# Performance work log

Hardware: AMD Instinct MI355X
Metric: run time of the kernel (lower is better)

The kernel has to match this reference:

```python
import jax, jax.numpy as jnp
import numpy as np

B, N, D, H = 4, 2048, 256, 4
DH = D // H
EPS = 1e-5


def setup_inputs() -> dict:
    key = jax.random.key(0)
    ks = jax.random.split(key, 12)
    s = 0.02
    return {
        "x0": jax.random.normal(ks[0], (B, N, D), jnp.float32),
        "x1": jax.random.normal(ks[1], (B, N, D), jnp.float32),
        "w_qk": jax.random.normal(ks[2], (D, D), jnp.float32) * s,
        "b_qk": jax.random.normal(ks[3], (D,), jnp.float32) * s,
        "w_v": jax.random.normal(ks[4], (D, D), jnp.float32) * s,
        "b_v": jax.random.normal(ks[5], (D,), jnp.float32) * s,
        "w_out": jax.random.normal(ks[6], (D, D), jnp.float32) * s,
        "b_out": jax.random.normal(ks[7], (D,), jnp.float32) * s,
        "w_f1": jax.random.normal(ks[8], (2 * D, 2 * D), jnp.float32) * s,
        "b_f1": jax.random.normal(ks[9], (2 * D,), jnp.float32) * s,
        "ln_g": jnp.ones((2 * D,), jnp.float32),
        "ln_b": jnp.zeros((2 * D,), jnp.float32),
        "w_f2": jax.random.normal(ks[10], (2 * D, D), jnp.float32) * s,
        "b_f2": jax.random.normal(ks[11], (D,), jnp.float32) * s,
    }


def _split_heads(t):  # [b, n, h*d] -> [b, h, n, d]
    b, n, _ = t.shape
    return t.reshape(b, n, H, DH).transpose(0, 2, 1, 3)


def _merge_heads(t):  # [b, h, n, d] -> [b, n, h*d]
    b, h, n, d = t.shape
    return t.transpose(0, 2, 1, 3).reshape(b, n, h * d)


def _layernorm(x, g, b):
    mu = jnp.mean(x, axis=-1, keepdims=True)
    var = jnp.mean(jnp.square(x - mu), axis=-1, keepdims=True)
    return (x - mu) * jax.lax.rsqrt(var + EPS) * g + b


def reference(x0, x1, w_qk, b_qk, w_v, b_v, w_out, b_out,
              w_f1, b_f1, ln_g, ln_b, w_f2, b_f2):
    scale = DH ** -0.5
    qk0 = _split_heads(x0 @ w_qk + b_qk) * scale ** 0.5
    qk1 = _split_heads(x1 @ w_qk + b_qk) * scale ** 0.5
    v0 = _split_heads(x0 @ w_v + b_v)
    v1 = _split_heads(x1 @ w_v + b_v)

    # shared similarity matrix, bisoftmax: row-softmax for 0->1, col-softmax for 1->0
    sim = jnp.einsum('bhid,bhjd->bhij', qk0, qk1)  # [b,h,n0,n1]
    a0 = jax.nn.softmax(sim, axis=-1)              # over n1
    a1 = jax.nn.softmax(sim, axis=-2)              # over n0
    m0 = jnp.einsum('bhij,bhjd->bhid', a0, v1)     # [b,h,n0,d]
    m1 = jnp.einsum('bhji,bhjd->bhid', a1, v0)     # [b,h,n1,d]

    m0 = _merge_heads(m0) @ w_out + b_out
    m1 = _merge_heads(m1) @ w_out + b_out

    def ffn(x, m):
        h = jnp.concatenate([x, m], axis=-1) @ w_f1 + b_f1
        h = jax.nn.gelu(_layernorm(h, ln_g, ln_b), approximate=False)
        return x + h @ w_f2 + b_f2

    return ffn(x0, m0), ffn(x1, m1)
```

## Files before the change

kernel.cpp:

```cpp
#include <hip/hip_runtime.h>
#include <cstdint>
#include <cstddef>


#define QKS2 0.4246609001440095f

typedef short bf16x8 __attribute__((ext_vector_type(8)));
typedef float f32x4  __attribute__((ext_vector_type(4)));
typedef float f32x16 __attribute__((ext_vector_type(16)));

__device__ __forceinline__ uint16_t f2bf(float f){
  union { float f; uint32_t u; } v; v.f = f;
  uint32_t r = v.u + 0x7FFFu + ((v.u >> 16) & 1u);
  return (uint16_t)(r >> 16);
}
__device__ __forceinline__ uint16_t f2bf_trunc(float f){
  union { float f; uint32_t u; } v; v.f = f;
  return (uint16_t)(v.u >> 16);
}
__device__ __forceinline__ float bf2f(uint16_t h){
  union { uint32_t u; float f; } v; v.u = ((uint32_t)h) << 16; return v.f;
}

__device__ __forceinline__ void gl_lds16(const void* g, void* l){
  void* g2 = const_cast<void*>(g);
  __builtin_amdgcn_global_load_lds((__attribute__((address_space(1))) void*)g2,
                                   (__attribute__((address_space(3))) void*)l,
                                   16, 0, 0);
}

__global__ __launch_bounds__(256) void conv_x_k(const float* __restrict__ x0,
                                                const float* __restrict__ x1,
                                                uint16_t* __restrict__ xb){
  const float* src = blockIdx.z ? x1 : x0;
  uint16_t* dst = xb + (size_t)blockIdx.z * 2097152;
  size_t i = ((size_t)blockIdx.x * 256 + threadIdx.x) * 4;
  float4 v = *(const float4*)(src + i);
  uint2 o;
  o.x = (uint32_t)f2bf(v.x) | ((uint32_t)f2bf(v.y) << 16);
  o.y = (uint32_t)f2bf(v.z) | ((uint32_t)f2bf(v.w) << 16);
  *(uint2*)(dst + i) = o;
}

__global__ __launch_bounds__(256) void conv_w_k(
    const float* w0, const float* w1, const float* w2, const float* w3, const float* w4,
    uint16_t* t0, uint16_t* t1, uint16_t* t2, uint16_t* t3, uint16_t* t4){
  const int z = blockIdx.z;
  const float* src = z==0? w0 : z==1? w1 : z==2? w2 : z==3? w3 : w4;
  uint16_t*   dst  = z==0? t0 : z==1? t1 : z==2? t2 : z==3? t3 : t4;
  const int K = (z>=3)? 512 : 256;
  const int N = (z==3)? 512 : 256;
  int idx = blockIdx.x * 256 + threadIdx.x;
  if (idx >= (K*N)/4) return;
  int k = idx / (N/4);
  int n = (idx % (N/4)) * 4;
  float4 v = *(const float4*)(src + (size_t)k*N + n);
  dst[(size_t)(n+0)*K + k] = f2bf(v.x);
  dst[(size_t)(n+1)*K + k] = f2bf(v.y);
  dst[(size_t)(n+2)*K + k] = f2bf(v.z);
  dst[(size_t)(n+3)*K + k] = f2bf(v.w);
}

struct GemmArgs {
  const uint16_t* A0; const uint16_t* A1;
  const uint16_t* A2_0; const uint16_t* A2_1;
  const uint16_t* Wt0; const uint16_t* Wt1;
  const float* bias0; const float* bias1;
  uint16_t* out0; uint16_t* out1; uint16_t* out2; uint16_t* out3;
  float* fout; const float* xf0; const float* xf1;
  int K;
};

template<int MODE>
__global__ __launch_bounds__(256, 4) void gemm_k(GemmArgs a){
  __shared__ __align__(16) uint16_t As[64*64];
  __shared__ __align__(16) uint16_t Bs[128*64];
  const int tid = threadIdx.x;
  const int w = tid >> 6, l = tid & 63;
  const int z = blockIdx.z;
  const int which = (MODE==0) ? (z & 1) : z;
  const int wsel  = (MODE==0) ? (z >> 1) : 0;
  const int K = a.K;
  const int m0 = blockIdx.x * 64;
  const int n0 = blockIdx.y * 128;
  const uint16_t* Wt   = wsel ? a.Wt1 : a.Wt0;
  const float* bias    = wsel ? a.bias1 : a.bias0;
  const uint16_t* Ab   = which ? a.A1 : a.A0;
  const uint16_t* Ab2  = which ? a.A2_1 : a.A2_0;

  f32x4 acc[4][2];
  #pragma unroll
  for (int i=0;i<4;++i)
    #pragma unroll
    for (int j=0;j<2;++j) acc[i][j] = (f32x4){0.f,0.f,0.f,0.f};

  const int lrow8 = l >> 3, lch = l & 7;
  const int swch = (lch ^ lrow8) * 8;
  const int quad = l >> 4, l15 = l & 15, h7 = l15 & 7;

  for (int k0 = 0; k0 < K; k0 += 64){
    __syncthreads();
    const uint16_t* Asrc; int lda;
    if (MODE == 2){
      Asrc = (k0 < 256) ? (Ab + k0) : (Ab2 + (k0 - 256));
      lda = 256;
    } else { Asrc = Ab + k0; lda = K; }
    #pragma unroll
    for (int j=0;j<2;++j){
      int wi = w*2 + j;
      int row = wi*8 + lrow8;
      gl_lds16(Asrc + (size_t)(m0 + row)*lda + swch, &As[wi*512]);
    }
    #pragma unroll
    for (int j=0;j<4;++j){
      int wi = w*4 + j;
      int row = wi*8 + lrow8;
      gl_lds16(Wt + (size_t)(n0 + row)*K + k0 + swch, &Bs[wi*512]);
    }
    __syncthreads();
    #pragma unroll
    for (int kc=0;kc<2;++kc){
      const int fch = ((kc*4 + quad) ^ h7) * 8;
      bf16x8 af[4], bfr[2];
      #pragma unroll
      for (int rt=0;rt<4;++rt)
        af[rt] = *(const bf16x8*)&As[(rt*16 + l15)*64 + fch];
      #pragma unroll
      for (int ct=0;ct<2;++ct)
        bfr[ct] = *(const bf16x8*)&Bs[(w*32 + ct*16 + l15)*64 + fch];
      #pragma unroll
      for (int rt=0;rt<4;++rt)
        #pragma unroll
        for (int ct=0;ct<2;++ct)
          acc[rt][ct] = __builtin_amdgcn_mfma_f32_16x16x32_bf16(af[rt], bfr[ct], acc[rt][ct], 0,0,0);
    }
  }

  #pragma unroll
  for (int rt=0;rt<4;++rt){
    const int r0 = m0 + rt*16 + (quad<<2);
    #pragma unroll
    for (int ct=0;ct<2;++ct){
      const int c = n0 + w*32 + ct*16 + l15;
      const float bv = bias[c];
      if (MODE == 0){
        if (wsel == 0){
          uint16_t* q = which ? a.out1 : a.out0;
          #pragma unroll
          for (int i=0;i<4;++i)
            q[(size_t)(r0+i)*256 + c] = f2bf((acc[rt][ct][i] + bv) * QKS2);
        } else {
          uint16_t* vt = which ? a.out3 : a.out2;
          const int bb = r0 >> 11, nn = r0 & 2047;
          const int hh = c >> 6,  dd = c & 63;
          uint2 pk;
          pk.x = (uint32_t)f2bf(acc[rt][ct][0] + bv) | ((uint32_t)f2bf(acc[rt][ct][1] + bv) << 16);
          pk.y = (uint32_t)f2bf(acc[rt][ct][2] + bv) | ((uint32_t)f2bf(acc[rt][ct][3] + bv) << 16);
          *(uint2*)(vt + ((size_t)((bb*4 + hh)*64 + dd))*2048 + nn) = pk;
        }
      } else if (MODE == 1){
        uint16_t* o = which ? a.out1 : a.out0;
        #pragma unroll
        for (int i=0;i<4;++i)
          o[(size_t)(r0+i)*256 + c] = f2bf(acc[rt][ct][i] + bv);
      } else if (MODE == 2){
        uint16_t* o = which ? a.out1 : a.out0;
        #pragma unroll
        for (int i=0;i<4;++i)
          o[(size_t)(r0+i)*512 + c] = f2bf(acc[rt][ct][i] + bv);
      } else {
        const float* xf = which ? a.xf1 : a.xf0;
        float* fo = a.fout + (size_t)which * 2097152;
        #pragma unroll
        for (int i=0;i<4;++i)
          fo[(size_t)(r0+i)*256 + c] = acc[rt][ct][i] + bv + xf[(size_t)(r0+i)*256 + c];
      }
    }
  }
}

__global__ __launch_bounds__(128, 2) void flash_k(
    const uint16_t* __restrict__ qk0, const uint16_t* __restrict__ qk1,
    const uint16_t* __restrict__ vt0, const uint16_t* __restrict__ vt1,
    uint16_t* __restrict__ m0b, uint16_t* __restrict__ m1b){
  __shared__ __align__(16) uint16_t Ks[64*64];
  __shared__ __align__(16) uint16_t Vs[64*64];
  __shared__ __align__(16) uint16_t Ps[64*64];
  const int tid = threadIdx.x;
  const int w = tid >> 6, l = tid & 63;
  const int qt = blockIdx.x;
  const int bh = blockIdx.y;
  const int dir = blockIdx.z;
  const int b = bh >> 2, h = bh & 3;
  const uint16_t* Q   = dir ? qk1 : qk0;
  const uint16_t* Kg  = dir ? qk0 : qk1;
  const uint16_t* Vt  = dir ? vt0 : vt1;
  uint16_t* outp      = dir ? m1b : m0b;

  const int qrow0 = b*2048 + qt*64;
  const int lrow8 = l >> 3, lch = l & 7;
  const int l31 = l & 31, lhi = l >> 5;
  const int rsub = l31 >> 3;

  const short ONE = (short)0x3F80;
  const bf16x8 ones = {ONE,ONE,ONE,ONE,ONE,ONE,ONE,ONE};

  #pragma unroll
  for (int j=0;j<4;++j){
    int g = w*4 + j;
    int row = g*8 + lrow8;
    int sc = (lch ^ lrow8 ^ (g & 7)) * 8;
    gl_lds16(Q + (size_t)(qrow0 + row)*256 + h*64 + sc, &Ps[g*512]);
  }
  __syncthreads();
  bf16x8 qf[4];
  {
    const int qmask = (l & 7) ^ ((w*4 + rsub) & 7);
    #pragma unroll
    for (int ks=0;ks<4;++ks){
      int ch = (ks*2 + lhi) ^ qmask;
      qf[ks] = *(const bf16x8*)&Ps[(w*32 + l31)*64 + ch*8];
    }
  }

  f32x16 o0, o1, lacc;
  #pragma unroll
  for (int i=0;i<16;++i){ o0[i]=0.f; o1[i]=0.f; lacc[i]=0.f; }

  const size_t vbase = (size_t)bh * 64 * 2048;
  const int pmask = (l & 7) ^ ((w*4 + rsub) & 7);

  for (int kt=0; kt<32; ++kt){
    __syncthreads();
    #pragma unroll
    for (int j=0;j<4;++j){
      int g = w*4 + j;
      int row = g*8 + lrow8;
      int sc = (lch ^ lrow8 ^ (g & 7)) * 8;
      gl_lds16(Kg + (size_t)(b*2048 + kt*64 + row)*256 + h*64 + sc, &Ks[g*512]);
      gl_lds16(Vt + vbase + (size_t)row*2048 + kt*64 + sc, &Vs[g*512]);
    }
    __syncthreads();

    f32x16 s0, s1;
    #pragma unroll
    for (int i=0;i<16;++i){ s0[i]=0.f; s1[i]=0.f; }
    #pragma unroll
    for (int ks=0;ks<4;++ks){
      int ch0 = ((ks*2 + lhi) ^ (l & 7) ^ rsub) * 8;
      int ch1 = ((ks*2 + lhi) ^ (l & 7) ^ (4 + rsub)) * 8;
      bf16x8 k0 = *(const bf16x8*)&Ks[l31*64 + ch0];
      bf16x8 k1 = *(const bf16x8*)&Ks[(32 + l31)*64 + ch1];
      s0 = __builtin_amdgcn_mfma_f32_32x32x16_bf16(qf[ks], k0, s0, 0,0,0);
      s1 = __builtin_amdgcn_mfma_f32_32x32x16_bf16(qf[ks], k1, s1, 0,0,0);
    }

    #pragma unroll
    for (int reg=0; reg<16; ++reg){
      int rm   = (reg&3) + 8*(reg>>2) + 4*lhi;
      int row  = w*32 + rm;
      int mask = ((rm & 7) ^ ((w*4 + (reg>>2)) & 7));
      int kc0  = (l31 >> 3);
      float p0 = __builtin_amdgcn_exp2f(s0[reg]);
      Ps[row*64 + ((kc0 ^ mask))*8 + (l31 & 7)] = f2bf_trunc(p0);
      float p1 = __builtin_amdgcn_exp2f(s1[reg]);
      Ps[row*64 + (((4 + kc0) ^ mask))*8 + (l31 & 7)] = f2bf_trunc(p1);
    }

    bf16x8 pf[4];
    #pragma unroll
    for (int ks=0;ks<4;++ks){
      int ch = ((ks*2 + lhi) ^ pmask) * 8;
      pf[ks] = *(const bf16x8*)&Ps[(w*32 + l31)*64 + ch];
    }
    #pragma unroll
    for (int ks=0;ks<4;++ks)
      lacc = __builtin_amdgcn_mfma_f32_32x32x16_bf16(pf[ks], ones, lacc, 0,0,0);
    #pragma unroll
    for (int ks=0;ks<4;++ks){
      int ch0 = ((ks*2 + lhi) ^ (l & 7) ^ rsub) * 8;
      int ch1 = ((ks*2 + lhi) ^ (l & 7) ^ (4 + rsub)) * 8;
      bf16x8 v0 = *(const bf16x8*)&Vs[l31*64 + ch0];
      bf16x8 v1 = *(const bf16x8*)&Vs[(32 + l31)*64 + ch1];
      o0 = __builtin_amdgcn_mfma_f32_32x32x16_bf16(pf[ks], v0, o0, 0,0,0);
      o1 = __builtin_amdgcn_mfma_f32_32x32x16_bf16(pf[ks], v1, o1, 0,0,0);
    }
  }

  const int c0 = h*64 + l31;
  #pragma unroll
  for (int reg=0; reg<16; ++reg){
    float inv = 1.0f / lacc[reg];
    int rm  = (reg&3) + 8*(reg>>2) + 4*lhi;
    size_t row = (size_t)(qrow0 + w*32 + rm);
    outp[row*256 + c0]      = f2bf(o0[reg] * inv);
    outp[row*256 + c0 + 32] = f2bf(o1[reg] * inv);
  }
}

__global__ __launch_bounds__(256) void lngelu_k(const uint16_t* __restrict__ hpre,
                                                const float* __restrict__ g,
                                                const float* __restrict__ bb,
                                                uint16_t* __restrict__ h){
  const int row = blockIdx.x*4 + (threadIdx.x >> 6);
  const int l = threadIdx.x & 63;
  const uint16_t* rp = hpre + (size_t)row*512 + l*8;
  uint4 raw = *(const uint4*)rp;
  uint32_t wv[4] = {raw.x, raw.y, raw.z, raw.w};
  float x[8];
  #pragma unroll
  for (int j=0;j<4;++j){
    x[2*j]   = bf2f((uint16_t)(wv[j] & 0xFFFFu));
    x[2*j+1] = bf2f((uint16_t)(wv[j] >> 16));
  }
  float s = 0.f;
  #pragma unroll
  for (int j=0;j<8;++j) s += x[j];
  #pragma unroll
  for (int off=1; off<64; off<<=1) s += __shfl_xor(s, off, 64);
  float mu = s * (1.0f/512.0f);
  float vs = 0.f;
  #pragma unroll
  for (int j=0;j<8;++j){ float d = x[j]-mu; vs += d*d; }
  #pragma unroll
  for (int off=1; off<64; off<<=1) vs += __shfl_xor(vs, off, 64);
  float rstd = rsqrtf(vs*(1.0f/512.0f) + 1e-5f);
  const float* gp = g + l*8;
  const float* bp = bb + l*8;
  uint32_t ow[4];
  #pragma unroll
  for (int j=0;j<4;++j){
    float y0 = (x[2*j]-mu)*rstd*gp[2*j] + bp[2*j];
    float y1 = (x[2*j+1]-mu)*rstd*gp[2*j+1] + bp[2*j+1];
    float g0 = 0.5f*y0*(1.0f + erff(y0*0.70710678118f));
    float g1 = 0.5f*y1*(1.0f + erff(y1*0.70710678118f));
    ow[j] = (uint32_t)f2bf(g0) | ((uint32_t)f2bf(g1) << 16);
  }
  uint4 out4 = {ow[0], ow[1], ow[2], ow[3]};
  *(uint4*)(h + (size_t)row*512 + l*8) = out4;
}

extern "C" void kernel_launch(void* const* d_in, const int* in_sizes, int n_in,
                              void* d_out, int out_size, void* d_ws, size_t ws_size,
                              hipStream_t stream){
  (void)in_sizes; (void)n_in; (void)out_size; (void)ws_size;
  const float* x0   = (const float*)d_in[0];
  const float* x1   = (const float*)d_in[1];
  const float* w_qk = (const float*)d_in[2];
  const float* b_qk = (const float*)d_in[3];
  const float* w_v  = (const float*)d_in[4];
  const float* b_v  = (const float*)d_in[5];
  const float* w_out= (const float*)d_in[6];
  const float* b_out= (const float*)d_in[7];
  const float* w_f1 = (const float*)d_in[8];
  const float* b_f1 = (const float*)d_in[9];
  const float* ln_g = (const float*)d_in[10];
  const float* ln_b = (const float*)d_in[11];
  const float* w_f2 = (const float*)d_in[12];
  const float* b_f2 = (const float*)d_in[13];

  char* ws = (char*)d_ws;
  uint16_t* xb    = (uint16_t*)(ws);
  uint16_t* wqkT  = (uint16_t*)(ws +  8388608);
  uint16_t* wvT   = (uint16_t*)(ws +  8519680);
  uint16_t* woutT = (uint16_t*)(ws +  8650752);
  uint16_t* wf1T  = (uint16_t*)(ws +  8781824);
  uint16_t* wf2T  = (uint16_t*)(ws +  9306112);
  uint16_t* qk0b  = (uint16_t*)(ws +  9568256);
  uint16_t* qk1b  = (uint16_t*)(ws + 13762560);
  uint16_t* vt0b  = (uint16_t*)(ws + 17956864);
  uint16_t* vt1b  = (uint16_t*)(ws + 22151168);
  uint16_t* m0b   = (uint16_t*)(ws + 26345472);
  uint16_t* m1b   = (uint16_t*)(ws + 30539776);
  uint16_t* mp0b  = (uint16_t*)(ws + 34734080);
  uint16_t* mp1b  = (uint16_t*)(ws + 38928384);
  uint16_t* hpreb = qk0b;
  uint16_t* hb    = m0b;

  conv_x_k<<<dim3(2048,1,2), 256, 0, stream>>>(x0, x1, xb);
  conv_w_k<<<dim3(256,1,5), 256, 0, stream>>>(w_qk, w_v, w_out, w_f1, w_f2,
                                              wqkT, wvT, woutT, wf1T, wf2T);

  GemmArgs g0 = {};
  g0.A0 = xb; g0.A1 = xb + 2097152;
  g0.Wt0 = wqkT; g0.Wt1 = wvT;
  g0.bias0 = b_qk; g0.bias1 = b_v;
  g0.out0 = qk0b; g0.out1 = qk1b; g0.out2 = vt0b; g0.out3 = vt1b;
  g0.K = 256;
  gemm_k<0><<<dim3(128,2,4), 256, 0, stream>>>(g0);

  flash_k<<<dim3(32,16,2), 128, 0, stream>>>(qk0b, qk1b, vt0b, vt1b, m0b, m1b);

  GemmArgs g1 = {};
  g1.A0 = m0b; g1.A1 = m1b;
  g1.Wt0 = woutT; g1.bias0 = b_out;
  g1.out0 = mp0b; g1.out1 = mp1b;
  g1.K = 256;
  gemm_k<1><<<dim3(128,2,2), 256, 0, stream>>>(g1);

  GemmArgs g2 = {};
  g2.A0 = xb; g2.A1 = xb + 2097152;
  g2.A2_0 = mp0b; g2.A2_1 = mp1b;
  g2.Wt0 = wf1T; g2.bias0 = b_f1;
  g2.out0 = hpreb; g2.out1 = hpreb + 4194304;
  g2.K = 512;
  gemm_k<2><<<dim3(128,4,2), 256, 0, stream>>>(g2);

  lngelu_k<<<dim3(4096,1,1), 256, 0, stream>>>(hpreb, ln_g, ln_b, hb);

  GemmArgs g3 = {};
  g3.A0 = hb; g3.A1 = hb + 4194304;
  g3.Wt0 = wf2T; g3.bias0 = b_f2;
  g3.fout = (float*)d_out;
  g3.xf0 = x0; g3.xf1 = x1;
  g3.K = 512;
  gemm_k<3><<<dim3(128,2,2), 256, 0, stream>>>(g3);
}
```

Baseline: 221.8 us.

## Compute transposed S^T in flash kernel, keep P in registers via bpermute, drop LDS

The attention kernel now computes S^T = K·Q^T so each lane holds scores for its own query column. The probabilities are repacked into MFMA operand fragments with ds_bpermute in place of a round trip through shared memory, and O^T is accumulated as V^T·P^T. K and V tiles are loaded straight from global memory into registers, with no LDS staging and no __syncthreads. This removes LDS traffic and barriers, but every wave now loads K/V itself with no sharing across the block, and the 16-byte gathers are strided.

```diff
diff --git a/kernel.cpp b/kernel.cpp
--- a/kernel.cpp
+++ b/kernel.cpp
@@ -14,12 +14,14 @@
   uint32_t r = v.u + 0x7FFFu + ((v.u >> 16) & 1u);
   return (uint16_t)(r >> 16);
 }
-__device__ __forceinline__ uint16_t f2bf_trunc(float f){
-  union { float f; uint32_t u; } v; v.f = f;
-  return (uint16_t)(v.u >> 16);
-}
 __device__ __forceinline__ float bf2f(uint16_t h){
   union { uint32_t u; float f; } v; v.u = ((uint32_t)h) << 16; return v.f;
+}
+__device__ __forceinline__ uint32_t fbits(float f){
+  union { float f; uint32_t u; } v; v.f = f; return v.u;
+}
+__device__ __forceinline__ uint32_t pk2bf(float a, float b){
+  return (fbits(b) & 0xFFFF0000u) | (fbits(a) >> 16);
 }
 
 __device__ __forceinline__ void gl_lds16(const void* g, void* l){
@@ -183,11 +185,9 @@
     const uint16_t* __restrict__ qk0, const uint16_t* __restrict__ qk1,
     const uint16_t* __restrict__ vt0, const uint16_t* __restrict__ vt1,
     uint16_t* __restrict__ m0b, uint16_t* __restrict__ m1b){
-  __shared__ __align__(16) uint16_t Ks[64*64];
-  __shared__ __align__(16) uint16_t Vs[64*64];
-  __shared__ __align__(16) uint16_t Ps[64*64];
   const int tid = threadIdx.x;
   const int w = tid >> 6, l = tid & 63;
+  const int l31 = l & 31, lhi = l >> 5;
   const int qt = blockIdx.x;
   const int bh = blockIdx.y;
   const int dir = blockIdx.z;
@@ -197,104 +197,105 @@
   const uint16_t* Vt  = dir ? vt0 : vt1;
   uint16_t* outp      = dir ? m1b : m0b;
 
-  const int qrow0 = b*2048 + qt*64;
-  const int lrow8 = l >> 3, lch = l & 7;
-  const int l31 = l & 31, lhi = l >> 5;
-  const int rsub = l31 >> 3;
+  const int qrow = b*2048 + qt*64 + w*32 + l31;
+  const int pidx = (l ^ 32) << 2;
+  const bool hi = (lhi != 0);
 
   const short ONE = (short)0x3F80;
   const bf16x8 ones = {ONE,ONE,ONE,ONE,ONE,ONE,ONE,ONE};
 
-  #pragma unroll
-  for (int j=0;j<4;++j){
-    int g = w*4 + j;
-    int row = g*8 + lrow8;
-    int sc = (lch ^ lrow8 ^ (g & 7)) * 8;
-    gl_lds16(Q + (size_t)(qrow0 + row)*256 + h*64 + sc, &Ps[g*512]);
-  }
-  __syncthreads();
   bf16x8 qf[4];
   {
-    const int qmask = (l & 7) ^ ((w*4 + rsub) & 7);
+    const uint16_t* qp = Q + (size_t)qrow*256 + h*64 + lhi*8;
+    #pragma unroll
+    for (int ks=0;ks<4;++ks) qf[ks] = *(const bf16x8*)(qp + ks*16);
+  }
+
+  f32x16 o0, o1, lacc;
+  #pragma unroll
+  for (int i=0;i<16;++i){ o0[i]=0.f; o1[i]=0.f; lacc[i]=0.f; }
+
+  const uint16_t* Kbase = Kg + (size_t)(b*2048 + l31)*256 + h*64 + lhi*8;
+  const uint16_t* Vbase = Vt + (size_t)bh*131072 + (size_t)l31*2048 + lhi*8;
+
+  for (int kt=0; kt<32; ++kt){
+    bf16x8 kf[2][4], vf[2][4];
+    #pragma unroll
+    for (int kb=0;kb<2;++kb)
+      #pragma unroll
+      for (int ks=0;ks<4;++ks)
+        kf[kb][ks] = *(const bf16x8*)(Kbase + (size_t)(kt*64 + kb*32)*256 + ks*16);
+    #pragma unroll
+    for (int db=0;db<2;++db)
+      #pragma unroll
+      for (int ks=0;ks<4;++ks)
+        vf[db][ks] = *(const bf16x8*)(Vbase + (size_t)db*32*2048 + kt*64 + ks*16);
+
+    f32x16 st0, st1;
+    #pragma unroll
+    for (int i=0;i<16;++i){ st0[i]=0.f; st1[i]=0.f; }
     #pragma unroll
     for (int ks=0;ks<4;++ks){
-      int ch = (ks*2 + lhi) ^ qmask;
-      qf[ks] = *(const bf16x8*)&Ps[(w*32 + l31)*64 + ch*8];
-    }
-  }
-
-  f32x16 o0, o1, lacc;
-  #pragma unroll
-  for (int i=0;i<16;++i){ o0[i]=0.f; o1[i]=0.f; lacc[i]=0.f; }
-
-  const size_t vbase = (size_t)bh * 64 * 2048;
-  const int pmask = (l & 7) ^ ((w*4 + rsub) & 7);
-
-  for (int kt=0; kt<32; ++kt){
-    __syncthreads();
-    #pragma unroll
-    for (int j=0;j<4;++j){
-      int g = w*4 + j;
-      int row = g*8 + lrow8;
-      int sc = (lch ^ lrow8 ^ (g & 7)) * 8;
-      gl_lds16(Kg + (size_t)(b*2048 + kt*64 + row)*256 + h*64 + sc, &Ks[g*512]);
-      gl_lds16(Vt + vbase + (size_t)row*2048 + kt*64 + sc, &Vs[g*512]);
-    }
-    __syncthreads();
-
-    f32x16 s0, s1;
-    #pragma unroll
-    for (int i=0;i<16;++i){ s0[i]=0.f; s1[i]=0.f; }
-    #pragma unroll
-    for (int ks=0;ks<4;++ks){
-      int ch0 = ((ks*2 + lhi) ^ (l & 7) ^ rsub) * 8;
-      int ch1 = ((ks*2 + lhi) ^ (l & 7) ^ (4 + rsub)) * 8;
-      bf16x8 k0 = *(const bf16x8*)&Ks[l31*64 + ch0];
-      bf16x8 k1 = *(const bf16x8*)&Ks[(32 + l31)*64 + ch1];
-      s0 = __builtin_amdgcn_mfma_f32_32x32x16_bf16(qf[ks], k0, s0, 0,0,0);
-      s1 = __builtin_amdgcn_mfma_f32_32x32x16_bf16(qf[ks], k1, s1, 0,0,0);
-    }
-
-    #pragma unroll
-    for (int reg=0; reg<16; ++reg){
-      int rm   = (reg&3) + 8*(reg>>2) + 4*lhi;
-      int row  = w*32 + rm;
-      int mask = ((rm & 7) ^ ((w*4 + (reg>>2)) & 7));
-      int kc0  = (l31 >> 3);
-      float p0 = __builtin_amdgcn_exp2f(s0[reg]);
-      Ps[row*64 + ((kc0 ^ mask))*8 + (l31 & 7)] = f2bf_trunc(p0);
-      float p1 = __builtin_amdgcn_exp2f(s1[reg]);
-      Ps[row*64 + (((4 + kc0) ^ mask))*8 + (l31 & 7)] = f2bf_trunc(p1);
-    }
-
-    bf16x8 pf[4];
-    #pragma unroll
-    for (int ks=0;ks<4;++ks){
-      int ch = ((ks*2 + lhi) ^ pmask) * 8;
-      pf[ks] = *(const bf16x8*)&Ps[(w*32 + l31)*64 + ch];
-    }
-    #pragma unroll
-    for (int ks=0;ks<4;++ks)
-      lacc = __builtin_amdgcn_mfma_f32_32x32x16_bf16(pf[ks], ones, lacc, 0,0,0);
-    #pragma unroll
-    for (int ks=0;ks<4;++ks){
-      int ch0 = ((ks*2 + lhi) ^ (l & 7) ^ rsub) * 8;
-      int ch1 = ((ks*2 + lhi) ^ (l & 7) ^ (4 + rsub)) * 8;
-      bf16x8 v0 = *(const bf16x8*)&Vs[l31*64 + ch0];
-      bf16x8 v1 = *(const bf16x8*)&Vs[(32 + l31)*64 + ch1];
-      o0 = __builtin_amdgcn_mfma_f32_32x32x16_bf16(pf[ks], v0, o0, 0,0,0);
-      o1 = __builtin_amdgcn_mfma_f32_32x32x16_bf16(pf[ks], v1, o1, 0,0,0);
-    }
-  }
-
-  const int c0 = h*64 + l31;
-  #pragma unroll
-  for (int reg=0; reg<16; ++reg){
-    float inv = 1.0f / lacc[reg];
-    int rm  = (reg&3) + 8*(reg>>2) + 4*lhi;
-    size_t row = (size_t)(qrow0 + w*32 + rm);
-    outp[row*256 + c0]      = f2bf(o0[reg] * inv);
-    outp[row*256 + c0 + 32] = f2bf(o1[reg] * inv);
+      st0 = __builtin_amdgcn_mfma_f32_32x32x16_bf16(kf[0][ks], qf[ks], st0, 0,0,0);
+      st1 = __builtin_amdgcn_mfma_f32_32x32x16_bf16(kf[1][ks], qf[ks], st1, 0,0,0);
+    }
+
+    uint32_t pkA[2][4], pkB[2][4];
+    #pragma unroll
+    for (int g=0; g<4; ++g){
+      float a0 = __builtin_amdgcn_exp2f(st0[4*g+0]);
+      float a1 = __builtin_amdgcn_exp2f(st0[4*g+1]);
+      float a2 = __builtin_amdgcn_exp2f(st0[4*g+2]);
+      float a3 = __builtin_amdgcn_exp2f(st0[4*g+3]);
+      pkA[0][g] = pk2bf(a0, a1);
+      pkB[0][g] = pk2bf(a2, a3);
+      float c0 = __builtin_amdgcn_exp2f(st1[4*g+0]);
+      float c1 = __builtin_amdgcn_exp2f(st1[4*g+1]);
+      float c2 = __builtin_amdgcn_exp2f(st1[4*g+2]);
+      float c3 = __builtin_amdgcn_exp2f(st1[4*g+3]);
+      pkA[1][g] = pk2bf(c0, c1);
+      pkB[1][g] = pk2bf(c2, c3);
+    }
+
+    bf16x8 pfrag[4];
+    #pragma unroll
+    for (int f=0; f<4; ++f){
+      const int sb = f >> 1, m2 = f & 1;
+      uint32_t ownA0 = pkA[sb][2*m2],   ownB0 = pkB[sb][2*m2];
+      uint32_t ownA1 = pkA[sb][2*m2+1], ownB1 = pkB[sb][2*m2+1];
+      uint32_t tA = hi ? ownA0 : ownA1;
+      uint32_t tB = hi ? ownB0 : ownB1;
+      uint32_t rA = (uint32_t)__builtin_amdgcn_ds_bpermute(pidx, (int)tA);
+      uint32_t rB = (uint32_t)__builtin_amdgcn_ds_bpermute(pidx, (int)tB);
+      uint32_t v0 = hi ? rA : ownA0;
+      uint32_t v1 = hi ? rB : ownB0;
+      uint32_t v2 = hi ? ownA1 : rA;
+      uint32_t v3 = hi ? ownB1 : rB;
+      union { uint32_t u[4]; bf16x8 v; } cvt;
+      cvt.u[0]=v0; cvt.u[1]=v1; cvt.u[2]=v2; cvt.u[3]=v3;
+      pfrag[f] = cvt.v;
+    }
+
+    #pragma unroll
+    for (int f=0; f<4; ++f)
+      lacc = __builtin_amdgcn_mfma_f32_32x32x16_bf16(ones, pfrag[f], lacc, 0,0,0);
+    #pragma unroll
+    for (int f=0; f<4; ++f){
+      o0 = __builtin_amdgcn_mfma_f32_32x32x16_bf16(vf[0][f], pfrag[f], o0, 0,0,0);
+      o1 = __builtin_amdgcn_mfma_f32_32x32x16_bf16(vf[1][f], pfrag[f], o1, 0,0,0);
+    }
+  }
+
+  const float inv = 1.0f / lacc[0];
+  uint16_t* op = outp + (size_t)qrow*256 + h*64 + lhi*4;
+  #pragma unroll
+  for (int g=0; g<4; ++g){
+    uint32_t p01 = (uint32_t)f2bf(o0[4*g+0]*inv) | ((uint32_t)f2bf(o0[4*g+1]*inv) << 16);
+    uint32_t p23 = (uint32_t)f2bf(o0[4*g+2]*inv) | ((uint32_t)f2bf(o0[4*g+3]*inv) << 16);
+    *(uint2*)(op + 8*g) = (uint2){p01, p23};
+    uint32_t q01 = (uint32_t)f2bf(o1[4*g+0]*inv) | ((uint32_t)f2bf(o1[4*g+1]*inv) << 16);
+    uint32_t q23 = (uint32_t)f2bf(o1[4*g+2]*inv) | ((uint32_t)f2bf(o1[4*g+3]*inv) << 16);
+    *(uint2*)(op + 32 + 8*g) = (uint2){q01, q23};
   }
 }
 
```

Result: slower. 299.7 us (+35.1%).

## Double K-tile depth in GEMM and flash kernels, merge conversion launches

Applied to the files above, without the earlier changes.

The GEMM now stages 128-wide K slices per iteration with a 16-chunk XOR swizzle, which halves the number of barrier-separated load/compute rounds, and its occupancy hint drops from 4 to 3 blocks. The flash kernel processes 128 keys per tile, computing four 32-key score blocks and then running one fused P·V and row-sum loop, so it has half as many sync rounds. The x and weight conversion kernels become a single launch with seven z-slices. In exchange LDS use per block rises, which may lower occupancy, and the conversion grid launches many idle weight blocks that exit early.

```diff
diff --git a/kernel.cpp b/kernel.cpp
--- a/kernel.cpp
+++ b/kernel.cpp
@@ -29,23 +29,23 @@
                                    16, 0, 0);
 }
 
-__global__ __launch_bounds__(256) void conv_x_k(const float* __restrict__ x0,
-                                                const float* __restrict__ x1,
-                                                uint16_t* __restrict__ xb){
-  const float* src = blockIdx.z ? x1 : x0;
-  uint16_t* dst = xb + (size_t)blockIdx.z * 2097152;
-  size_t i = ((size_t)blockIdx.x * 256 + threadIdx.x) * 4;
-  float4 v = *(const float4*)(src + i);
-  uint2 o;
-  o.x = (uint32_t)f2bf(v.x) | ((uint32_t)f2bf(v.y) << 16);
-  o.y = (uint32_t)f2bf(v.z) | ((uint32_t)f2bf(v.w) << 16);
-  *(uint2*)(dst + i) = o;
-}
-
-__global__ __launch_bounds__(256) void conv_w_k(
+__global__ __launch_bounds__(256) void conv_all_k(
+    const float* __restrict__ x0, const float* __restrict__ x1,
+    uint16_t* __restrict__ xb,
     const float* w0, const float* w1, const float* w2, const float* w3, const float* w4,
     uint16_t* t0, uint16_t* t1, uint16_t* t2, uint16_t* t3, uint16_t* t4){
   const int z = blockIdx.z;
+  if (z >= 5){
+    const float* src = (z == 6) ? x1 : x0;
+    uint16_t* dst = xb + (size_t)(z - 5) * 2097152;
+    size_t i = ((size_t)blockIdx.x * 256 + threadIdx.x) * 4;
+    float4 v = *(const float4*)(src + i);
+    uint2 o;
+    o.x = (uint32_t)f2bf(v.x) | ((uint32_t)f2bf(v.y) << 16);
+    o.y = (uint32_t)f2bf(v.z) | ((uint32_t)f2bf(v.w) << 16);
+    *(uint2*)(dst + i) = o;
+    return;
+  }
   const float* src = z==0? w0 : z==1? w1 : z==2? w2 : z==3? w3 : w4;
   uint16_t*   dst  = z==0? t0 : z==1? t1 : z==2? t2 : z==3? t3 : t4;
   const int K = (z>=3)? 512 : 256;
@@ -72,9 +72,9 @@
 };
 
 template<int MODE>
-__global__ __launch_bounds__(256, 4) void gemm_k(GemmArgs a){
-  __shared__ __align__(16) uint16_t As[64*64];
-  __shared__ __align__(16) uint16_t Bs[128*64];
+__global__ __launch_bounds__(256, 3) void gemm_k(GemmArgs a){
+  __shared__ __align__(16) uint16_t As[64*128];
+  __shared__ __align__(16) uint16_t Bs[128*128];
   const int tid = threadIdx.x;
   const int w = tid >> 6, l = tid & 63;
   const int z = blockIdx.z;
@@ -94,11 +94,10 @@
     #pragma unroll
     for (int j=0;j<2;++j) acc[i][j] = (f32x4){0.f,0.f,0.f,0.f};
 
-  const int lrow8 = l >> 3, lch = l & 7;
-  const int swch = (lch ^ lrow8) * 8;
-  const int quad = l >> 4, l15 = l & 15, h7 = l15 & 7;
-
-  for (int k0 = 0; k0 < K; k0 += 64){
+  const int lrow16 = l >> 4, lch16 = l & 15;
+  const int quad = l >> 4, l15 = l & 15;
+
+  for (int k0 = 0; k0 < K; k0 += 128){
     __syncthreads();
     const uint16_t* Asrc; int lda;
     if (MODE == 2){
@@ -106,28 +105,30 @@
       lda = 256;
     } else { Asrc = Ab + k0; lda = K; }
     #pragma unroll
-    for (int j=0;j<2;++j){
-      int wi = w*2 + j;
-      int row = wi*8 + lrow8;
-      gl_lds16(Asrc + (size_t)(m0 + row)*lda + swch, &As[wi*512]);
-    }
-    #pragma unroll
     for (int j=0;j<4;++j){
-      int wi = w*4 + j;
-      int row = wi*8 + lrow8;
-      gl_lds16(Wt + (size_t)(n0 + row)*K + k0 + swch, &Bs[wi*512]);
+      int g = w*4 + j;
+      int row = g*4 + lrow16;
+      int sc = lch16 ^ (row & 15);
+      gl_lds16(Asrc + (size_t)(m0 + row)*lda + sc*8, &As[g*512]);
+    }
+    #pragma unroll
+    for (int j=0;j<8;++j){
+      int g = w*8 + j;
+      int row = g*4 + lrow16;
+      int sc = lch16 ^ (row & 15);
+      gl_lds16(Wt + (size_t)(n0 + row)*K + k0 + sc*8, &Bs[g*512]);
     }
     __syncthreads();
     #pragma unroll
-    for (int kc=0;kc<2;++kc){
-      const int fch = ((kc*4 + quad) ^ h7) * 8;
+    for (int kc=0;kc<4;++kc){
+      const int ch = kc*4 + quad;
       bf16x8 af[4], bfr[2];
       #pragma unroll
       for (int rt=0;rt<4;++rt)
-        af[rt] = *(const bf16x8*)&As[(rt*16 + l15)*64 + fch];
+        af[rt] = *(const bf16x8*)&As[(rt*16 + l15)*128 + (ch ^ l15)*8];
       #pragma unroll
       for (int ct=0;ct<2;++ct)
-        bfr[ct] = *(const bf16x8*)&Bs[(w*32 + ct*16 + l15)*64 + fch];
+        bfr[ct] = *(const bf16x8*)&Bs[(w*32 + ct*16 + l15)*128 + (ch ^ l15)*8];
       #pragma unroll
       for (int rt=0;rt<4;++rt)
         #pragma unroll
@@ -183,11 +184,13 @@
     const uint16_t* __restrict__ qk0, const uint16_t* __restrict__ qk1,
     const uint16_t* __restrict__ vt0, const uint16_t* __restrict__ vt1,
     uint16_t* __restrict__ m0b, uint16_t* __restrict__ m1b){
-  __shared__ __align__(16) uint16_t Ks[64*64];
-  __shared__ __align__(16) uint16_t Vs[64*64];
-  __shared__ __align__(16) uint16_t Ps[64*64];
+  __shared__ __align__(16) uint16_t Ks[128*64];
+  __shared__ __align__(16) uint16_t Vs[64*128];
+  __shared__ __align__(16) uint16_t Ps[64*128];
   const int tid = threadIdx.x;
   const int w = tid >> 6, l = tid & 63;
+  const int l31 = l & 31, lhi = l >> 5;
+  const int rsub = l31 >> 3;
   const int qt = blockIdx.x;
   const int bh = blockIdx.y;
   const int dir = blockIdx.z;
@@ -198,9 +201,8 @@
   uint16_t* outp      = dir ? m1b : m0b;
 
   const int qrow0 = b*2048 + qt*64;
-  const int lrow8 = l >> 3, lch = l & 7;
-  const int l31 = l & 31, lhi = l >> 5;
-  const int rsub = l31 >> 3;
+  const int lrow8 = l >> 3, lch8 = l & 7;
+  const int lrow16 = l >> 4, lch16 = l & 15;
 
   const short ONE = (short)0x3F80;
   const bf16x8 ones = {ONE,ONE,ONE,ONE,ONE,ONE,ONE,ONE};
@@ -209,81 +211,70 @@
   for (int j=0;j<4;++j){
     int g = w*4 + j;
     int row = g*8 + lrow8;
-    int sc = (lch ^ lrow8 ^ (g & 7)) * 8;
-    gl_lds16(Q + (size_t)(qrow0 + row)*256 + h*64 + sc, &Ps[g*512]);
+    int sc = lch8 ^ lrow8 ^ (g & 7);
+    gl_lds16(Q + (size_t)(qrow0 + row)*256 + h*64 + sc*8, &Ps[g*512]);
   }
   __syncthreads();
   bf16x8 qf[4];
   {
     const int qmask = (l & 7) ^ ((w*4 + rsub) & 7);
     #pragma unroll
-    for (int ks=0;ks<4;++ks){
-      int ch = (ks*2 + lhi) ^ qmask;
-      qf[ks] = *(const bf16x8*)&Ps[(w*32 + l31)*64 + ch*8];
-    }
+    for (int ks=0;ks<4;++ks)
+      qf[ks] = *(const bf16x8*)&Ps[(w*32 + l31)*64 + (((ks*2 + lhi) ^ qmask))*8];
   }
 
   f32x16 o0, o1, lacc;
   #pragma unroll
   for (int i=0;i<16;++i){ o0[i]=0.f; o1[i]=0.f; lacc[i]=0.f; }
 
-  const size_t vbase = (size_t)bh * 64 * 2048;
-  const int pmask = (l & 7) ^ ((w*4 + rsub) & 7);
-
-  for (int kt=0; kt<32; ++kt){
+  const size_t vbase = (size_t)bh * 131072;
+  const int pm15 = l31 & 15;
+
+  for (int kt=0; kt<16; ++kt){
     __syncthreads();
     #pragma unroll
-    for (int j=0;j<4;++j){
-      int g = w*4 + j;
-      int row = g*8 + lrow8;
-      int sc = (lch ^ lrow8 ^ (g & 7)) * 8;
-      gl_lds16(Kg + (size_t)(b*2048 + kt*64 + row)*256 + h*64 + sc, &Ks[g*512]);
-      gl_lds16(Vt + vbase + (size_t)row*2048 + kt*64 + sc, &Vs[g*512]);
+    for (int j=0;j<8;++j){
+      int g = w*8 + j;
+      int rowk = g*8 + lrow8;
+      int sck = lch8 ^ lrow8 ^ (g & 7);
+      gl_lds16(Kg + (size_t)(b*2048 + kt*128 + rowk)*256 + h*64 + sck*8, &Ks[g*512]);
+      int rowv = g*4 + lrow16;
+      int scv = lch16 ^ (rowv & 15);
+      gl_lds16(Vt + vbase + (size_t)rowv*2048 + kt*128 + scv*8, &Vs[g*1024]);
     }
     __syncthreads();
 
-    f32x16 s0, s1;
-    #pragma unroll
-    for (int i=0;i<16;++i){ s0[i]=0.f; s1[i]=0.f; }
-    #pragma unroll
-    for (int ks=0;ks<4;++ks){
-      int ch0 = ((ks*2 + lhi) ^ (l & 7) ^ rsub) * 8;
-      int ch1 = ((ks*2 + lhi) ^ (l & 7) ^ (4 + rsub)) * 8;
-      bf16x8 k0 = *(const bf16x8*)&Ks[l31*64 + ch0];
-      bf16x8 k1 = *(const bf16x8*)&Ks[(32 + l31)*64 + ch1];
-      s0 = __builtin_amdgcn_mfma_f32_32x32x16_bf16(qf[ks], k0, s0, 0,0,0);
-      s1 = __builtin_amdgcn_mfma_f32_32x32x16_bf16(qf[ks], k1, s1, 0,0,0);
-    }
-
-    #pragma unroll
-    for (int reg=0; reg<16; ++reg){
-      int rm   = (reg&3) + 8*(reg>>2) + 4*lhi;
-      int row  = w*32 + rm;
-      int mask = ((rm & 7) ^ ((w*4 + (reg>>2)) & 7));
-      int kc0  = (l31 >> 3);
-      float p0 = __builtin_amdgcn_exp2f(s0[reg]);
-      Ps[row*64 + ((kc0 ^ mask))*8 + (l31 & 7)] = f2bf_trunc(p0);
-      float p1 = __builtin_amdgcn_exp2f(s1[reg]);
-      Ps[row*64 + (((4 + kc0) ^ mask))*8 + (l31 & 7)] = f2bf_trunc(p1);
-    }
-
-    bf16x8 pf[4];
-    #pragma unroll
-    for (int ks=0;ks<4;++ks){
-      int ch = ((ks*2 + lhi) ^ pmask) * 8;
-      pf[ks] = *(const bf16x8*)&Ps[(w*32 + l31)*64 + ch];
-    }
-    #pragma unroll
-    for (int ks=0;ks<4;++ks)
-      lacc = __builtin_amdgcn_mfma_f32_32x32x16_bf16(pf[ks], ones, lacc, 0,0,0);
-    #pragma unroll
-    for (int ks=0;ks<4;++ks){
-      int ch0 = ((ks*2 + lhi) ^ (l & 7) ^ rsub) * 8;
-      int ch1 = ((ks*2 + lhi) ^ (l & 7) ^ (4 + rsub)) * 8;
-      bf16x8 v0 = *(const bf16x8*)&Vs[l31*64 + ch0];
-      bf16x8 v1 = *(const bf16x8*)&Vs[(32 + l31)*64 + ch1];
-      o0 = __builtin_amdgcn_mfma_f32_32x32x16_bf16(pf[ks], v0, o0, 0,0,0);
-      o1 = __builtin_amdgcn_mfma_f32_32x32x16_bf16(pf[ks], v1, o1, 0,0,0);
+    #pragma unroll
+    for (int kb=0;kb<4;++kb){
+      const int kmask = (l31 & 7) ^ ((kb*4 + rsub) & 7);
+      f32x16 st;
+      #pragma unroll
+      for (int i=0;i<16;++i) st[i]=0.f;
+      #pragma unroll
+      for (int ks=0;ks<4;++ks){
+        bf16x8 kf = *(const bf16x8*)&Ks[(kb*32 + l31)*64 + (((ks*2 + lhi) ^ kmask))*8];
+        st = __builtin_amdgcn_mfma_f32_32x32x16_bf16(qf[ks], kf, st, 0,0,0);
+      }
+      const int kc = kb*4 + rsub;
+      #pragma unroll
+      for (int reg=0; reg<16; ++reg){
+        int qrm  = (reg&3) + 8*(reg>>2) + 4*lhi;
+        int prow = w*32 + qrm;
+        int slot = kc ^ (qrm & 15);
+        float p = __builtin_amdgcn_exp2f(st[reg]);
+        Ps[prow*128 + slot*8 + (l31 & 7)] = f2bf_trunc(p);
+      }
+    }
+
+    #pragma unroll
+    for (int f=0; f<8; ++f){
+      const int slot = ((f*2 + lhi) ^ pm15) * 8;
+      bf16x8 pf = *(const bf16x8*)&Ps[(w*32 + l31)*128 + slot];
+      bf16x8 v0 = *(const bf16x8*)&Vs[l31*128 + slot];
+      bf16x8 v1 = *(const bf16x8*)&Vs[(32 + l31)*128 + slot];
+      lacc = __builtin_amdgcn_mfma_f32_32x32x16_bf16(pf, ones, lacc, 0,0,0);
+      o0 = __builtin_amdgcn_mfma_f32_32x32x16_bf16(pf, v0, o0, 0,0,0);
+      o1 = __builtin_amdgcn_mfma_f32_32x32x16_bf16(pf, v1, o1, 0,0,0);
     }
   }
 
@@ -291,8 +282,8 @@
   #pragma unroll
   for (int reg=0; reg<16; ++reg){
     float inv = 1.0f / lacc[reg];
-    int rm  = (reg&3) + 8*(reg>>2) + 4*lhi;
-    size_t row = (size_t)(qrow0 + w*32 + rm);
+    int qrm = (reg&3) + 8*(reg>>2) + 4*lhi;
+    size_t row = (size_t)(qrow0 + w*32 + qrm);
     outp[row*256 + c0]      = f2bf(o0[reg] * inv);
     outp[row*256 + c0 + 32] = f2bf(o1[reg] * inv);
   }
@@ -377,9 +368,8 @@
   uint16_t* hpreb = qk0b;
   uint16_t* hb    = m0b;
 
-  conv_x_k<<<dim3(2048,1,2), 256, 0, stream>>>(x0, x1, xb);
-  conv_w_k<<<dim3(256,1,5), 256, 0, stream>>>(w_qk, w_v, w_out, w_f1, w_f2,
-                                              wqkT, wvT, woutT, wf1T, wf2T);
+  conv_all_k<<<dim3(2048,1,7), 256, 0, stream>>>(x0, x1, xb,
+      w_qk, w_v, w_out, w_f1, w_f2, wqkT, wvT, woutT, wf1T, wf2T);
 
   GemmArgs g0 = {};
   g0.A0 = xb; g0.A1 = xb + 2097152;
```

New measurement: 248.1 us. 1.12x slower.
